# Kernel tuning notes

Measured on AMD Instinct MI355X. Metric: run time of the kernel, lower is better.

Reference implementation:

```python
import jax, jax.numpy as jnp
import numpy as np


def log_g(x):
    # faithful to torch: where(x>=0, log(relu(x)+0.5), 5 - softplus(-x))
    return jnp.where(x >= 0, jnp.log(jax.nn.relu(x) + 0.5), 5.0 - jax.nn.softplus(-x))


def setup_inputs() -> dict:
    key = jax.random.key(0)
    ks = jax.random.split(key, 6)
    B, T, D, H = 8, 4096, 1024, 1024
    s = 1.0 / np.sqrt(D)
    return {
        "x": jax.random.normal(ks[0], (B, T, D), jnp.float32),
        "h_0": jax.random.normal(ks[1], (B, 1, H), jnp.float32),
        "Wz_w": jax.random.normal(ks[2], (D, H), jnp.float32) * s,
        "Wz_b": jax.random.normal(ks[3], (H,), jnp.float32) * 0.1,
        "Wh_w": jax.random.normal(ks[4], (D, H), jnp.float32) * s,
        "Wh_b": jax.random.normal(ks[5], (H,), jnp.float32) * 0.1,
    }


def reference(x, h_0, Wz_w, Wz_b, Wh_w, Wh_b):
    # k = W_z(x)
    k = jnp.einsum('btd,dh->bth', x, Wz_w) + Wz_b
    log_z = -jax.nn.softplus(-k)          # log sigmoid(k)
    log_coeffs = -jax.nn.softplus(k)      # log(1 - sigmoid(k))
    log_h0 = log_g(h_0)                                            # [B,1,H]
    log_tilde_h = log_g(jnp.einsum('btd,dh->bth', x, Wh_w) + Wh_b)  # [B,T,H]
    log_values = jnp.concatenate([log_h0, log_z + log_tilde_h], axis=1)  # [B,T+1,H]
    # a_star = pad(cumsum(log_coeffs, dim=1), (0,0,1,0)) -> one zero row at t=0
    a_star = jnp.pad(jnp.cumsum(log_coeffs, axis=1), ((0, 0), (1, 0), (0, 0)))  # [B,T+1,H]
    log_h = a_star + jax.lax.cumlogsumexp(log_values - a_star, axis=1)
    return jnp.exp(log_h)[:, 1:]  # [B,T,H]
```

## Files before the change

### kernel.cpp

```cpp
#include <hip/hip_runtime.h>
#include <hip/hip_bf16.h>
#include <stdint.h>

#define B_   8
#define T_   4096
#define D_   1024
#define H_   1024
#define M_   (B_ * T_)
#define NC_  64
#define TC_  64


typedef __attribute__((ext_vector_type(4))) float f32x4;
typedef __attribute__((ext_vector_type(8))) short bfr8;
typedef _Float16 f16;
typedef __attribute__((ext_vector_type(2))) _Float16 f16x2;

__device__ __forceinline__ unsigned short f2bf(float f) {
  unsigned int u = __float_as_uint(f);
  u += 0x7fffu + ((u >> 16) & 1u);
  return (unsigned short)(u >> 16);
}
__device__ __forceinline__ float bf2f(unsigned short h) {
  return __uint_as_float(((unsigned int)h) << 16);
}

__device__ __forceinline__ void gload16(const void* g, void* l) {
  __builtin_amdgcn_global_load_lds((const __attribute__((address_space(1))) void*)g,
                                   (__attribute__((address_space(3))) void*)l,
                                   16, 0, 0);
}

__device__ __forceinline__ float g_of(float hv) {
  return (hv >= 0.f) ? (hv + 0.5f)
                     : 148.4131591025766f / (1.f + __expf(-hv));
}

__global__ void prep_w2(const float* __restrict__ Wz, const float* __restrict__ Wh,
                        unsigned short* __restrict__ wtp, float* __restrict__ whT,
                        unsigned int* __restrict__ fcnt)
{
  int kt = blockIdx.x;
  int nt = blockIdx.y;
  int m  = blockIdx.z;
  if (kt == 0 && nt == 0 && m == 0 && threadIdx.x == 0) *fcnt = 0u;
  __shared__ float tile[32][65];
  const float* W = m ? Wh : Wz;
  int n0 = nt * 64, k0 = kt * 32;
  int t = threadIdx.x;
  {
    int r = t >> 3, c0 = (t & 7) * 8;
    const float* src = &W[(size_t)(k0 + r) * 1024 + n0 + c0];
#pragma unroll
    for (int i = 0; i < 8; i++) tile[r][c0 + i] = src[i];
  }
  __syncthreads();
  unsigned short* out = wtp + ((size_t)(m * 16 + nt) * 32 + kt) * 4096;
  {
    int n = t >> 2;
    int cb = (t & 3) * 2;
    unsigned int u[8];
#pragma unroll
    for (int q = 0; q < 8; q++) {
      unsigned short w2[2];
#pragma unroll
      for (int h = 0; h < 2; h++) {
        int e = q * 2 + h;
        int c = cb + (e >> 3), el = e & 7;
        int s = c ^ (n & 7);
        float v = tile[(s & 3) * 8 + el][n];
        unsigned short hi = f2bf(v);
        w2[h] = (s < 4) ? hi : f2bf(v - bf2f(hi));
      }
      u[q] = (unsigned int)w2[0] | ((unsigned int)w2[1] << 16);
    }
    uint4* dst = (uint4*)&out[(size_t)n * 64 + cb * 8];
    dst[0] = make_uint4(u[0], u[1], u[2], u[3]);
    dst[1] = make_uint4(u[4], u[5], u[6], u[7]);
  }
  if (m == 1) {
    int n = t >> 2, kk0 = (t & 3) * 8;
    float* dstf = &whT[(size_t)(n0 + n) * 1024 + k0 + kk0];
#pragma unroll
    for (int i = 0; i < 8; i++) dstf[i] = tile[kk0 + i][n];
  }
}

__global__ __launch_bounds__(256, 2) void gemm_cv(
    const float* __restrict__ x,
    const unsigned short* __restrict__ wtp,
    const float* __restrict__ bz, const float* __restrict__ bhb,
    f16x2* __restrict__ cvbuf,
    unsigned int* __restrict__ fcnt, unsigned int* __restrict__ flist,
    unsigned int fcap)
{
  __shared__ __align__(16) unsigned short Ac[2][8192];
  __shared__ __align__(16) unsigned short Bzs[2][4096];
  __shared__ __align__(16) unsigned short Bhs[2][4096];
  int tid = threadIdx.x;
  int lane = tid & 63, wv = tid >> 6;
  int wr = wv >> 1, wc = wv & 1;
  int lrow = lane & 15, lq = lane >> 4;

  int bid = blockIdx.x;
  int cpx = gridDim.x >> 3;
  int swz = (bid & 7) * cpx + (bid >> 3);
  int grp = swz >> 7, wi = swz & 127;
  int mt = grp * 8 + (wi & 7);
  int nt = wi >> 3;
  int m0 = mt * 128, n0 = nt * 64;

  f32x4 accz[4][2], acch[4][2];
#pragma unroll
  for (int i = 0; i < 4; i++)
#pragma unroll
    for (int j = 0; j < 2; j++) {
      accz[i][j] = (f32x4){0.f, 0.f, 0.f, 0.f};
      acch[i][j] = (f32x4){0.f, 0.f, 0.f, 0.f};
    }

  int art = tid >> 3, ac4 = (tid & 7) * 4;
  int awb = art * 64 + ((((ac4 >> 3) ^ (art & 7)) << 3) | (ac4 & 4));
  const float* xp = x + (size_t)(m0 + art) * D_ + ac4;

  int fch = (lq ^ (lrow & 7)) << 3;
  int aoff = (wr * 64 + lrow) * 64 + fch;
  int boff = (wc * 32 + lrow) * 64 + fch;

  const unsigned short* bsz = wtp + (size_t)nt * 131072 + tid * 8;
  const unsigned short* bsh = bsz + 2097152;

  uint4 xa[4];

  auto loadX = [&](int kt) {
#pragma unroll
    for (int p = 0; p < 4; p++)
      xa[p] = *(const uint4*)(xp + (size_t)p * 32 * D_ + kt * 32);
  };
  auto stageB = [&](int kt, int b) {
#pragma unroll
    for (int j = 0; j < 2; j++) {
      gload16(bsz + (size_t)kt * 4096 + j * 2048, &Bzs[b][j * 2048 + tid * 8]);
      gload16(bsh + (size_t)kt * 4096 + j * 2048, &Bhs[b][j * 2048 + tid * 8]);
    }
  };
  auto writeA = [&](int b) {
#pragma unroll
    for (int p = 0; p < 4; p++) {
      uint4 vu = xa[p];
      unsigned int hi01 = __builtin_amdgcn_perm(vu.y, vu.x, 0x07060302u);
      unsigned int hi23 = __builtin_amdgcn_perm(vu.w, vu.z, 0x07060302u);
      float l0 = __uint_as_float(vu.x) - __uint_as_float(vu.x & 0xffff0000u);
      float l1 = __uint_as_float(vu.y) - __uint_as_float(vu.y & 0xffff0000u);
      float l2 = __uint_as_float(vu.z) - __uint_as_float(vu.z & 0xffff0000u);
      float l3 = __uint_as_float(vu.w) - __uint_as_float(vu.w & 0xffff0000u);
      unsigned int lo01 = __builtin_amdgcn_perm(__float_as_uint(l1),
                                                __float_as_uint(l0), 0x07060302u);
      unsigned int lo23 = __builtin_amdgcn_perm(__float_as_uint(l3),
                                                __float_as_uint(l2), 0x07060302u);
      int bi = p * 2048 + awb;
      *(uint2*)&Ac[b][bi]      = make_uint2(hi01, hi23);
      *(uint2*)&Ac[b][bi ^ 32] = make_uint2(lo01, lo23);
    }
  };
  auto doMFMA = [&](int cur) {
    bfr8 ah[4], al[4], bzhv[2], bzlv[2], bhhv[2], bhlv[2];
#pragma unroll
    for (int f = 0; f < 4; f++) {
      ah[f] = *(const bfr8*)&Ac[cur][aoff + f * 1024];
      al[f] = *(const bfr8*)&Ac[cur][(aoff + f * 1024) ^ 32];
    }
#pragma unroll
    for (int j = 0; j < 2; j++) {
      bzhv[j] = *(const bfr8*)&Bzs[cur][boff + j * 1024];
      bzlv[j] = *(const bfr8*)&Bzs[cur][(boff + j * 1024) ^ 32];
      bhhv[j] = *(const bfr8*)&Bhs[cur][boff + j * 1024];
      bhlv[j] = *(const bfr8*)&Bhs[cur][(boff + j * 1024) ^ 32];
    }
#pragma unroll
    for (int i = 0; i < 4; i++)
#pragma unroll
      for (int j = 0; j < 2; j++) {
        accz[i][j] = __builtin_amdgcn_mfma_f32_16x16x32_bf16(ah[i], bzhv[j], accz[i][j], 0, 0, 0);
        accz[i][j] = __builtin_amdgcn_mfma_f32_16x16x32_bf16(al[i], bzhv[j], accz[i][j], 0, 0, 0);
        accz[i][j] = __builtin_amdgcn_mfma_f32_16x16x32_bf16(ah[i], bzlv[j], accz[i][j], 0, 0, 0);
        acch[i][j] = __builtin_amdgcn_mfma_f32_16x16x32_bf16(ah[i], bhhv[j], acch[i][j], 0, 0, 0);
        acch[i][j] = __builtin_amdgcn_mfma_f32_16x16x32_bf16(al[i], bhhv[j], acch[i][j], 0, 0, 0);
        acch[i][j] = __builtin_amdgcn_mfma_f32_16x16x32_bf16(ah[i], bhlv[j], acch[i][j], 0, 0, 0);
      }
  };

  loadX(0);
  stageB(0, 0);
  writeA(0);
  __syncthreads();

  auto step = [&](int kt, int cur, int nxt) {
    loadX(kt + 1);
    stageB(kt + 1, nxt);
    doMFMA(cur);
    writeA(nxt);
    __syncthreads();
  };

#pragma unroll 1
  for (int kt = 0; kt < 30; kt += 2) {
    step(kt, 0, 1);
    step(kt + 1, 1, 0);
  }
  step(30, 0, 1);
  doMFMA(1);

#pragma unroll
  for (int j = 0; j < 2; j++) {
    int col = n0 + wc * 32 + j * 16 + lrow;
    float kb = bz[col], hb = bhb[col];
#pragma unroll
    for (int i = 0; i < 4; i++) {
      int row0 = m0 + wr * 64 + i * 16 + lq * 4;
#pragma unroll
      for (int r = 0; r < 4; r++) {
        float kv = accz[i][j][r] + kb;
        float hv = acch[i][j][r] + hb;
        f16 kf = (f16)kv;
        float c  = 1.f / (1.f + __expf((float)kf));
        float v  = (1.f - c) * g_of(hv);
        size_t off = (size_t)(row0 + r) * H_ + col;
        f16x2 pr; pr[0] = kf; pr[1] = (f16)v;
        cvbuf[off] = pr;
        if (__builtin_fabsf(hv) < 1e-3f) {
          unsigned int p = atomicAdd(fcnt, 1u);
          if (p < fcap) flist[p] = (unsigned int)off;
        }
      }
    }
  }
}

__global__ void fixup_kc512(const float* __restrict__ x, const float* __restrict__ whT,
                            const float* __restrict__ bhb, f16x2* cvbuf,
                            const unsigned int* __restrict__ fcnt,
                            const unsigned int* __restrict__ flist, unsigned int fcap)
{
  unsigned int n = *fcnt; if (n > fcap) n = fcap;
  unsigned int gtid = blockIdx.x * blockDim.x + threadIdx.x;
  unsigned int nt = gridDim.x * blockDim.x;
  const unsigned int lim = (unsigned int)M_ * (unsigned int)H_;
  for (unsigned int i = gtid; i < n; i += nt) {
    unsigned int o = flist[i];
    if (o >= lim) continue;
    unsigned int row = o >> 10, col = o & 1023u;
    const float* xr = x + (size_t)row * D_;
    const float* wr = whT + (size_t)col * D_;
    float a1 = 0.f, a2 = 0.f;
    for (int d = 0; d < 512; d++)
      a1 = fmaf(xr[d], wr[d], a1);
    for (int d = 512; d < 1024; d++)
      a2 = fmaf(xr[d], wr[d], a2);
    float hs = (a1 + a2) + bhb[col];
    float g  = (hs >= 0.f) ? (hs + 0.5f)
                           : 148.4131591025766f / (1.f + __expf(-hs));
    f16x2 pr = cvbuf[o];
    float z  = 1.f / (1.f + __expf(-(float)pr[0]));
    pr[1] = (f16)(z * g);
    cvbuf[o] = pr;
  }
}

__global__ void scan_p1(const f16x2* __restrict__ cv,
                        float* __restrict__ Cc, float* __restrict__ Vv)
{
  int h = blockIdx.x * 256 + threadIdx.x;
  int ch = blockIdx.y, b = blockIdx.z;
  size_t base = ((size_t)b * T_ + (size_t)ch * TC_) * H_ + h;
  float C = 1.f, V = 0.f;
#pragma unroll 4
  for (int i = 0; i < TC_; i++) {
    f16x2 p = cv[base + (size_t)i * H_];
    float c = 1.f / (1.f + __expf((float)p[0]));
    V = fmaf(c, V, (float)p[1]);
    C *= c;
  }
  size_t o = ((size_t)b * NC_ + ch) * H_ + h;
  Cc[o] = C; Vv[o] = V;
}

__global__ void scan_p2(const float* __restrict__ h0, const float* __restrict__ Cc,
                        const float* __restrict__ Vv, float* __restrict__ Hi)
{
  int idx = blockIdx.x * 256 + threadIdx.x;
  float hs = g_of(h0[idx]);
  int b = idx >> 10, h = idx & 1023;
  for (int ch = 0; ch < NC_; ch++) {
    size_t o = ((size_t)b * NC_ + ch) * H_ + h;
    Hi[o] = hs;
    hs = fmaf(Cc[o], hs, Vv[o]);
  }
}

__global__ void scan_p3(void* buf, const float* __restrict__ Hi)
{
  __shared__ f16x2 S[TC_][256];
  const f16x2* cv = (const f16x2*)buf;
  float* out = (float*)buf;
  int t = threadIdx.x;
  int hg = blockIdx.x, ch = blockIdx.y, b = blockIdx.z;
  int col = hg * 256 + t;
  size_t base = ((size_t)b * T_ + (size_t)ch * TC_) * H_ + col;
#pragma unroll 4
  for (int r = 0; r < TC_; r++)
    S[r][t] = cv[base + (size_t)r * H_];
  __syncthreads();
  float hs = Hi[((size_t)b * NC_ + ch) * H_ + col];
#pragma unroll 4
  for (int r = 0; r < TC_; r++) {
    f16x2 p = S[r][t];
    float c = 1.f / (1.f + __expf((float)p[0]));
    hs = fmaf(c, hs, (float)p[1]);
    out[base + (size_t)r * H_] = hs;
  }
}

extern "C" void kernel_launch(void* const* d_in, const int* in_sizes, int n_in,
                              void* d_out, int out_size, void* d_ws, size_t ws_size,
                              hipStream_t stream)
{
  const float* x  = (const float*)d_in[0];
  const float* h0 = (const float*)d_in[1];
  const float* Wz = (const float*)d_in[2];
  const float* bz = (const float*)d_in[3];
  const float* Wh = (const float*)d_in[4];
  const float* bh = (const float*)d_in[5];
  char* ws = (char*)d_ws;

  const size_t MiB = 1024u * 1024u;
  unsigned int* fcnt  = (unsigned int*)(ws);
  unsigned int* flist = (unsigned int*)(ws + 4096);
  const unsigned int fcap = 250u * 1024u;
  unsigned short* wtp = (unsigned short*)(ws + 2 * MiB);
  float* Cc = (float*)(ws + 10 * MiB);
  float* Vv = (float*)(ws + 12 * MiB);
  float* Hi = (float*)(ws + 14 * MiB);
  float* whT = (float*)(ws + 16 * MiB);

  f16x2* cvbuf = (f16x2*)d_out;

  prep_w2<<<dim3(32, 16, 2), 256, 0, stream>>>(Wz, Wh, wtp, whT, fcnt);
  gemm_cv<<<4096, 256, 0, stream>>>(x, wtp, bz, bh, cvbuf, fcnt, flist, fcap);
  fixup_kc512<<<512, 256, 0, stream>>>(x, whT, bh, cvbuf, fcnt, flist, fcap);
  scan_p1<<<dim3(4, 64, 8), 256, 0, stream>>>(cvbuf, Cc, Vv);
  scan_p2<<<32, 256, 0, stream>>>(h0, Cc, Vv, Hi);
  scan_p3<<<dim3(4, 64, 8), 256, 0, stream>>>(d_out, Hi);
}
```

Measured before the change: 708.0 us.

## Enlarge GEMM block tile to 256x128 with 8 waves and raise MFMA priority

The main GEMM moves from 128x64 tiles with 4 waves to 256x128 tiles with 8 waves (512 threads). The weight prep kernel is reworked to emit matching 128-column packed tiles. The goal is more reuse of the split-bf16 A and B operands per LDS load and less global traffic per output element. The change also adds s_setprio around the MFMA loop and swaps __syncthreads for an explicit waitcnt plus barrier. In exchange it uses more LDS and accumulator registers per block, which may lower occupancy, and the grid shrinks to 1024 blocks.

```diff
diff --git a/kernel.cpp b/kernel.cpp
--- a/kernel.cpp
+++ b/kernel.cpp
@@ -44,49 +44,46 @@
   int nt = blockIdx.y;
   int m  = blockIdx.z;
   if (kt == 0 && nt == 0 && m == 0 && threadIdx.x == 0) *fcnt = 0u;
-  __shared__ float tile[32][65];
+  __shared__ float tile[32][129];
   const float* W = m ? Wh : Wz;
-  int n0 = nt * 64, k0 = kt * 32;
+  int n0 = nt * 128, k0 = kt * 32;
   int t = threadIdx.x;
   {
-    int r = t >> 3, c0 = (t & 7) * 8;
+    int r = t >> 3, c0 = (t & 7) * 16;
     const float* src = &W[(size_t)(k0 + r) * 1024 + n0 + c0];
 #pragma unroll
-    for (int i = 0; i < 8; i++) tile[r][c0 + i] = src[i];
+    for (int i = 0; i < 16; i++) tile[r][c0 + i] = src[i];
   }
   __syncthreads();
-  unsigned short* out = wtp + ((size_t)(m * 16 + nt) * 32 + kt) * 4096;
-  {
-    int n = t >> 2;
-    int cb = (t & 3) * 2;
-    unsigned int u[8];
-#pragma unroll
-    for (int q = 0; q < 8; q++) {
+  unsigned short* out = wtp + ((size_t)(m * 8 + nt) * 32 + kt) * 8192;
+  int n = t >> 1, hf = t & 1;
+#pragma unroll
+  for (int c4 = 0; c4 < 4; c4++) {
+    int c = hf * 4 + c4;
+    int s = c ^ (n & 7);
+    unsigned int u[4];
+#pragma unroll
+    for (int q = 0; q < 4; q++) {
       unsigned short w2[2];
 #pragma unroll
-      for (int h = 0; h < 2; h++) {
-        int e = q * 2 + h;
-        int c = cb + (e >> 3), el = e & 7;
-        int s = c ^ (n & 7);
-        float v = tile[(s & 3) * 8 + el][n];
+      for (int e2 = 0; e2 < 2; e2++) {
+        int e = q * 2 + e2;
+        float v = tile[(s & 3) * 8 + e][n];
         unsigned short hi = f2bf(v);
-        w2[h] = (s < 4) ? hi : f2bf(v - bf2f(hi));
+        w2[e2] = (s < 4) ? hi : f2bf(v - bf2f(hi));
       }
       u[q] = (unsigned int)w2[0] | ((unsigned int)w2[1] << 16);
     }
-    uint4* dst = (uint4*)&out[(size_t)n * 64 + cb * 8];
-    dst[0] = make_uint4(u[0], u[1], u[2], u[3]);
-    dst[1] = make_uint4(u[4], u[5], u[6], u[7]);
+    *(uint4*)&out[(size_t)n * 64 + c * 8] = make_uint4(u[0], u[1], u[2], u[3]);
   }
   if (m == 1) {
-    int n = t >> 2, kk0 = (t & 3) * 8;
-    float* dstf = &whT[(size_t)(n0 + n) * 1024 + k0 + kk0];
-#pragma unroll
-    for (int i = 0; i < 8; i++) dstf[i] = tile[kk0 + i][n];
-  }
-}
-
-__global__ __launch_bounds__(256, 2) void gemm_cv(
+#pragma unroll
+    for (int i = 0; i < 16; i++)
+      whT[(size_t)(n0 + n) * 1024 + k0 + hf * 16 + i] = tile[hf * 16 + i][n];
+  }
+}
+
+__global__ __launch_bounds__(512, 2) void gemm_cv(
     const float* __restrict__ x,
     const unsigned short* __restrict__ wtp,
     const float* __restrict__ bz, const float* __restrict__ bhb,
@@ -94,130 +91,162 @@
     unsigned int* __restrict__ fcnt, unsigned int* __restrict__ flist,
     unsigned int fcap)
 {
-  __shared__ __align__(16) unsigned short Ac[2][8192];
-  __shared__ __align__(16) unsigned short Bzs[2][4096];
-  __shared__ __align__(16) unsigned short Bhs[2][4096];
+  __shared__ __align__(16) unsigned short Ac[2][16384];
+  __shared__ __align__(16) unsigned short Bz[2][8192];
+  __shared__ __align__(16) unsigned short Bh[2][8192];
   int tid = threadIdx.x;
   int lane = tid & 63, wv = tid >> 6;
-  int wr = wv >> 1, wc = wv & 1;
+  int wm = wv >> 2, wn = wv & 3;
   int lrow = lane & 15, lq = lane >> 4;
 
   int bid = blockIdx.x;
   int cpx = gridDim.x >> 3;
   int swz = (bid & 7) * cpx + (bid >> 3);
-  int grp = swz >> 7, wi = swz & 127;
-  int mt = grp * 8 + (wi & 7);
-  int nt = wi >> 3;
-  int m0 = mt * 128, n0 = nt * 64;
-
-  f32x4 accz[4][2], acch[4][2];
-#pragma unroll
-  for (int i = 0; i < 4; i++)
+  int nt = swz & 7;
+  int mt = swz >> 3;
+  int m0 = mt * 256, n0 = nt * 128;
+
+  f32x4 accz[8][2], acch[8][2];
+#pragma unroll
+  for (int i = 0; i < 8; i++)
 #pragma unroll
     for (int j = 0; j < 2; j++) {
       accz[i][j] = (f32x4){0.f, 0.f, 0.f, 0.f};
       acch[i][j] = (f32x4){0.f, 0.f, 0.f, 0.f};
     }
 
-  int art = tid >> 3, ac4 = (tid & 7) * 4;
-  int awb = art * 64 + ((((ac4 >> 3) ^ (art & 7)) << 3) | (ac4 & 4));
-  const float* xp = x + (size_t)(m0 + art) * D_ + ac4;
+  int art = tid >> 1, half = tid & 1;
+  int r7 = art & 7;
+  int c0 = (((half * 2)     ) ^ r7) << 3;
+  int c1 = (((half * 2) + 1) ^ r7) << 3;
+  int abw = art * 64;
+  const float* xp = x + (size_t)(m0 + art) * D_ + half * 16;
 
   int fch = (lq ^ (lrow & 7)) << 3;
-  int aoff = (wr * 64 + lrow) * 64 + fch;
-  int boff = (wc * 32 + lrow) * 64 + fch;
-
-  const unsigned short* bsz = wtp + (size_t)nt * 131072 + tid * 8;
+  int abase = (wm * 128 + lrow) * 64 + fch;
+  int bbase = (wn * 32 + lrow) * 64 + fch;
+
+  const unsigned short* bsz = wtp + (size_t)nt * 262144;
   const unsigned short* bsh = bsz + 2097152;
 
   uint4 xa[4];
 
   auto loadX = [&](int kt) {
 #pragma unroll
-    for (int p = 0; p < 4; p++)
-      xa[p] = *(const uint4*)(xp + (size_t)p * 32 * D_ + kt * 32);
-  };
-  auto stageB = [&](int kt, int b) {
+    for (int q = 0; q < 4; q++)
+      xa[q] = *(const uint4*)(xp + (size_t)kt * 32 + q * 4);
+  };
+  auto stageB = [&](int kt, int nb) {
+    size_t o = (size_t)kt * 8192 + tid * 8;
+    gload16(bsz + o,        &Bz[nb][tid * 8]);
+    gload16(bsz + o + 4096, &Bz[nb][4096 + tid * 8]);
+    gload16(bsh + o,        &Bh[nb][tid * 8]);
+    gload16(bsh + o + 4096, &Bh[nb][4096 + tid * 8]);
+  };
+  auto writeA = [&](int nb) {
+    unsigned int h00 = __builtin_amdgcn_perm(xa[0].y, xa[0].x, 0x07060302u);
+    unsigned int h01 = __builtin_amdgcn_perm(xa[0].w, xa[0].z, 0x07060302u);
+    unsigned int h02 = __builtin_amdgcn_perm(xa[1].y, xa[1].x, 0x07060302u);
+    unsigned int h03 = __builtin_amdgcn_perm(xa[1].w, xa[1].z, 0x07060302u);
+    unsigned int h10 = __builtin_amdgcn_perm(xa[2].y, xa[2].x, 0x07060302u);
+    unsigned int h11 = __builtin_amdgcn_perm(xa[2].w, xa[2].z, 0x07060302u);
+    unsigned int h12 = __builtin_amdgcn_perm(xa[3].y, xa[3].x, 0x07060302u);
+    unsigned int h13 = __builtin_amdgcn_perm(xa[3].w, xa[3].z, 0x07060302u);
+    unsigned int l00, l01, l02, l03, l10, l11, l12, l13;
+    {
+      float a0 = __uint_as_float(xa[0].x) - __uint_as_float(xa[0].x & 0xffff0000u);
+      float a1 = __uint_as_float(xa[0].y) - __uint_as_float(xa[0].y & 0xffff0000u);
+      float a2 = __uint_as_float(xa[0].z) - __uint_as_float(xa[0].z & 0xffff0000u);
+      float a3 = __uint_as_float(xa[0].w) - __uint_as_float(xa[0].w & 0xffff0000u);
+      float b0 = __uint_as_float(xa[1].x) - __uint_as_float(xa[1].x & 0xffff0000u);
+      float b1 = __uint_as_float(xa[1].y) - __uint_as_float(xa[1].y & 0xffff0000u);
+      float b2 = __uint_as_float(xa[1].z) - __uint_as_float(xa[1].z & 0xffff0000u);
+      float b3 = __uint_as_float(xa[1].w) - __uint_as_float(xa[1].w & 0xffff0000u);
+      l00 = __builtin_amdgcn_perm(__float_as_uint(a1), __float_as_uint(a0), 0x07060302u);
+      l01 = __builtin_amdgcn_perm(__float_as_uint(a3), __float_as_uint(a2), 0x07060302u);
+      l02 = __builtin_amdgcn_perm(__float_as_uint(b1), __float_as_uint(b0), 0x07060302u);
+      l03 = __builtin_amdgcn_perm(__float_as_uint(b3), __float_as_uint(b2), 0x07060302u);
+    }
+    {
+      float a0 = __uint_as_float(xa[2].x) - __uint_as_float(xa[2].x & 0xffff0000u);
+      float a1 = __uint_as_float(xa[2].y) - __uint_as_float(xa[2].y & 0xffff0000u);
+      float a2 = __uint_as_float(xa[2].z) - __uint_as_float(xa[2].z & 0xffff0000u);
+      float a3 = __uint_as_float(xa[2].w) - __uint_as_float(xa[2].w & 0xffff0000u);
+      float b0 = __uint_as_float(xa[3].x) - __uint_as_float(xa[3].x & 0xffff0000u);
+      float b1 = __uint_as_float(xa[3].y) - __uint_as_float(xa[3].y & 0xffff0000u);
+      float b2 = __uint_as_float(xa[3].z) - __uint_as_float(xa[3].z & 0xffff0000u);
+      float b3 = __uint_as_float(xa[3].w) - __uint_as_float(xa[3].w & 0xffff0000u);
+      l10 = __builtin_amdgcn_perm(__float_as_uint(a1), __float_as_uint(a0), 0x07060302u);
+      l11 = __builtin_amdgcn_perm(__float_as_uint(a3), __float_as_uint(a2), 0x07060302u);
+      l12 = __builtin_amdgcn_perm(__float_as_uint(b1), __float_as_uint(b0), 0x07060302u);
+      l13 = __builtin_amdgcn_perm(__float_as_uint(b3), __float_as_uint(b2), 0x07060302u);
+    }
+    *(uint4*)&Ac[nb][abw + c0]        = make_uint4(h00, h01, h02, h03);
+    *(uint4*)&Ac[nb][abw + c1]        = make_uint4(h10, h11, h12, h13);
+    *(uint4*)&Ac[nb][(abw + c0) ^ 32] = make_uint4(l00, l01, l02, l03);
+    *(uint4*)&Ac[nb][(abw + c1) ^ 32] = make_uint4(l10, l11, l12, l13);
+  };
+  auto mfma_tile = [&](int cur) {
+    bfr8 bzh[2], bzl[2], bhh[2], bhl[2];
 #pragma unroll
     for (int j = 0; j < 2; j++) {
-      gload16(bsz + (size_t)kt * 4096 + j * 2048, &Bzs[b][j * 2048 + tid * 8]);
-      gload16(bsh + (size_t)kt * 4096 + j * 2048, &Bhs[b][j * 2048 + tid * 8]);
-    }
-  };
-  auto writeA = [&](int b) {
-#pragma unroll
-    for (int p = 0; p < 4; p++) {
-      uint4 vu = xa[p];
-      unsigned int hi01 = __builtin_amdgcn_perm(vu.y, vu.x, 0x07060302u);
-      unsigned int hi23 = __builtin_amdgcn_perm(vu.w, vu.z, 0x07060302u);
-      float l0 = __uint_as_float(vu.x) - __uint_as_float(vu.x & 0xffff0000u);
-      float l1 = __uint_as_float(vu.y) - __uint_as_float(vu.y & 0xffff0000u);
-      float l2 = __uint_as_float(vu.z) - __uint_as_float(vu.z & 0xffff0000u);
-      float l3 = __uint_as_float(vu.w) - __uint_as_float(vu.w & 0xffff0000u);
-      unsigned int lo01 = __builtin_amdgcn_perm(__float_as_uint(l1),
-                                                __float_as_uint(l0), 0x07060302u);
-      unsigned int lo23 = __builtin_amdgcn_perm(__float_as_uint(l3),
-                                                __float_as_uint(l2), 0x07060302u);
-      int bi = p * 2048 + awb;
-      *(uint2*)&Ac[b][bi]      = make_uint2(hi01, hi23);
-      *(uint2*)&Ac[b][bi ^ 32] = make_uint2(lo01, lo23);
-    }
-  };
-  auto doMFMA = [&](int cur) {
-    bfr8 ah[4], al[4], bzhv[2], bzlv[2], bhhv[2], bhlv[2];
-#pragma unroll
-    for (int f = 0; f < 4; f++) {
-      ah[f] = *(const bfr8*)&Ac[cur][aoff + f * 1024];
-      al[f] = *(const bfr8*)&Ac[cur][(aoff + f * 1024) ^ 32];
-    }
-#pragma unroll
-    for (int j = 0; j < 2; j++) {
-      bzhv[j] = *(const bfr8*)&Bzs[cur][boff + j * 1024];
-      bzlv[j] = *(const bfr8*)&Bzs[cur][(boff + j * 1024) ^ 32];
-      bhhv[j] = *(const bfr8*)&Bhs[cur][boff + j * 1024];
-      bhlv[j] = *(const bfr8*)&Bhs[cur][(boff + j * 1024) ^ 32];
-    }
-#pragma unroll
-    for (int i = 0; i < 4; i++)
+      int o = bbase + j * 1024;
+      bzh[j] = *(const bfr8*)&Bz[cur][o];
+      bzl[j] = *(const bfr8*)&Bz[cur][o ^ 32];
+      bhh[j] = *(const bfr8*)&Bh[cur][o];
+      bhl[j] = *(const bfr8*)&Bh[cur][o ^ 32];
+    }
+    __builtin_amdgcn_s_setprio(1);
+#pragma unroll
+    for (int i = 0; i < 8; i++) {
+      int o = abase + i * 1024;
+      bfr8 ah = *(const bfr8*)&Ac[cur][o];
+      bfr8 al = *(const bfr8*)&Ac[cur][o ^ 32];
 #pragma unroll
       for (int j = 0; j < 2; j++) {
-        accz[i][j] = __builtin_amdgcn_mfma_f32_16x16x32_bf16(ah[i], bzhv[j], accz[i][j], 0, 0, 0);
-        accz[i][j] = __builtin_amdgcn_mfma_f32_16x16x32_bf16(al[i], bzhv[j], accz[i][j], 0, 0, 0);
-        accz[i][j] = __builtin_amdgcn_mfma_f32_16x16x32_bf16(ah[i], bzlv[j], accz[i][j], 0, 0, 0);
-        acch[i][j] = __builtin_amdgcn_mfma_f32_16x16x32_bf16(ah[i], bhhv[j], acch[i][j], 0, 0, 0);
-        acch[i][j] = __builtin_amdgcn_mfma_f32_16x16x32_bf16(al[i], bhhv[j], acch[i][j], 0, 0, 0);
-        acch[i][j] = __builtin_amdgcn_mfma_f32_16x16x32_bf16(ah[i], bhlv[j], acch[i][j], 0, 0, 0);
+        accz[i][j] = __builtin_amdgcn_mfma_f32_16x16x32_bf16(ah, bzh[j], accz[i][j], 0, 0, 0);
+        accz[i][j] = __builtin_amdgcn_mfma_f32_16x16x32_bf16(al, bzh[j], accz[i][j], 0, 0, 0);
+        accz[i][j] = __builtin_amdgcn_mfma_f32_16x16x32_bf16(ah, bzl[j], accz[i][j], 0, 0, 0);
+        acch[i][j] = __builtin_amdgcn_mfma_f32_16x16x32_bf16(ah, bhh[j], acch[i][j], 0, 0, 0);
+        acch[i][j] = __builtin_amdgcn_mfma_f32_16x16x32_bf16(al, bhh[j], acch[i][j], 0, 0, 0);
+        acch[i][j] = __builtin_amdgcn_mfma_f32_16x16x32_bf16(ah, bhl[j], acch[i][j], 0, 0, 0);
       }
+    }
+    __builtin_amdgcn_s_setprio(0);
   };
 
   loadX(0);
   stageB(0, 0);
   writeA(0);
-  __syncthreads();
-
-  auto step = [&](int kt, int cur, int nxt) {
+  asm volatile("s_waitcnt vmcnt(0) lgkmcnt(0)" ::: "memory");
+  __builtin_amdgcn_sched_barrier(0);
+  __builtin_amdgcn_s_barrier();
+
+  auto kstep = [&](int kt, int cur) {
     loadX(kt + 1);
-    stageB(kt + 1, nxt);
-    doMFMA(cur);
-    writeA(nxt);
-    __syncthreads();
+    stageB(kt + 1, cur ^ 1);
+    mfma_tile(cur);
+    writeA(cur ^ 1);
+    asm volatile("s_waitcnt vmcnt(0) lgkmcnt(0)" ::: "memory");
+    __builtin_amdgcn_sched_barrier(0);
+    __builtin_amdgcn_s_barrier();
   };
 
 #pragma unroll 1
   for (int kt = 0; kt < 30; kt += 2) {
-    step(kt, 0, 1);
-    step(kt + 1, 1, 0);
-  }
-  step(30, 0, 1);
-  doMFMA(1);
+    kstep(kt, 0);
+    kstep(kt + 1, 1);
+  }
+  kstep(30, 0);
+  mfma_tile(1);
 
 #pragma unroll
   for (int j = 0; j < 2; j++) {
-    int col = n0 + wc * 32 + j * 16 + lrow;
+    int col = n0 + wn * 32 + j * 16 + lrow;
     float kb = bz[col], hb = bhb[col];
 #pragma unroll
-    for (int i = 0; i < 4; i++) {
-      int row0 = m0 + wr * 64 + i * 16 + lq * 4;
+    for (int i = 0; i < 8; i++) {
+      int row0 = m0 + wm * 128 + i * 16 + lq * 4;
 #pragma unroll
       for (int r = 0; r < 4; r++) {
         float kv = accz[i][j][r] + kb;
@@ -345,8 +374,8 @@
 
   f16x2* cvbuf = (f16x2*)d_out;
 
-  prep_w2<<<dim3(32, 16, 2), 256, 0, stream>>>(Wz, Wh, wtp, whT, fcnt);
-  gemm_cv<<<4096, 256, 0, stream>>>(x, wtp, bz, bh, cvbuf, fcnt, flist, fcap);
+  prep_w2<<<dim3(32, 8, 2), 256, 0, stream>>>(Wz, Wh, wtp, whT, fcnt);
+  gemm_cv<<<1024, 512, 0, stream>>>(x, wtp, bz, bh, cvbuf, fcnt, flist, fcap);
   fixup_kc512<<<512, 256, 0, stream>>>(x, whT, bh, cvbuf, fcnt, flist, fcap);
   scan_p1<<<dim3(4, 64, 8), 256, 0, stream>>>(cvbuf, Cc, Vv);
   scan_p2<<<32, 256, 0, stream>>>(h0, Cc, Vv, Hi);
```

Result: slower. 747.2 us (+5.5%).

## Replace double-buffered LDS pipeline with single buffer and two barriers per k-step

Applied to the files above, without the earlier changes.

The GEMM main loop drops its double-buffered shared-memory tiles for A and B in favor of single buffers, issuing B staging and the A write, syncing, prefetching the next X into registers, running MFMAs, then syncing again. This halves LDS use per block, which can allow more resident blocks per CU. In exchange it adds a second barrier per iteration and loses the overlap between filling the next buffer and computing on the current one, so global-to-LDS B loads are now exposed.

```diff
diff --git a/kernel.cpp b/kernel.cpp
--- a/kernel.cpp
+++ b/kernel.cpp
@@ -94,9 +94,9 @@
     unsigned int* __restrict__ fcnt, unsigned int* __restrict__ flist,
     unsigned int fcap)
 {
-  __shared__ __align__(16) unsigned short Ac[2][8192];
-  __shared__ __align__(16) unsigned short Bzs[2][4096];
-  __shared__ __align__(16) unsigned short Bhs[2][4096];
+  __shared__ __align__(16) unsigned short Ac[8192];
+  __shared__ __align__(16) unsigned short Bzs[4096];
+  __shared__ __align__(16) unsigned short Bhs[4096];
   int tid = threadIdx.x;
   int lane = tid & 63, wv = tid >> 6;
   int wr = wv >> 1, wc = wv & 1;
@@ -137,14 +137,14 @@
     for (int p = 0; p < 4; p++)
       xa[p] = *(const uint4*)(xp + (size_t)p * 32 * D_ + kt * 32);
   };
-  auto stageB = [&](int kt, int b) {
-#pragma unroll
-    for (int j = 0; j < 2; j++) {
-      gload16(bsz + (size_t)kt * 4096 + j * 2048, &Bzs[b][j * 2048 + tid * 8]);
-      gload16(bsh + (size_t)kt * 4096 + j * 2048, &Bhs[b][j * 2048 + tid * 8]);
-    }
+  auto stageB = [&](int kt) {
+    size_t o = (size_t)kt * 4096;
+    gload16(bsz + o,        &Bzs[tid * 8]);
+    gload16(bsz + o + 2048, &Bzs[2048 + tid * 8]);
+    gload16(bsh + o,        &Bhs[tid * 8]);
+    gload16(bsh + o + 2048, &Bhs[2048 + tid * 8]);
   };
-  auto writeA = [&](int b) {
+  auto writeA = [&]() {
 #pragma unroll
     for (int p = 0; p < 4; p++) {
       uint4 vu = xa[p];
@@ -159,57 +159,49 @@
       unsigned int lo23 = __builtin_amdgcn_perm(__float_as_uint(l3),
                                                 __float_as_uint(l2), 0x07060302u);
       int bi = p * 2048 + awb;
-      *(uint2*)&Ac[b][bi]      = make_uint2(hi01, hi23);
-      *(uint2*)&Ac[b][bi ^ 32] = make_uint2(lo01, lo23);
+      *(uint2*)&Ac[bi]      = make_uint2(hi01, hi23);
+      *(uint2*)&Ac[bi ^ 32] = make_uint2(lo01, lo23);
     }
   };
-  auto doMFMA = [&](int cur) {
-    bfr8 ah[4], al[4], bzhv[2], bzlv[2], bhhv[2], bhlv[2];
+  auto doMFMA = [&]() {
+    bfr8 ah[4], al[4], bzh[2], bzl[2], bhh[2], bhl[2];
 #pragma unroll
     for (int f = 0; f < 4; f++) {
-      ah[f] = *(const bfr8*)&Ac[cur][aoff + f * 1024];
-      al[f] = *(const bfr8*)&Ac[cur][(aoff + f * 1024) ^ 32];
+      int o = aoff + f * 1024;
+      ah[f] = *(const bfr8*)&Ac[o];
+      al[f] = *(const bfr8*)&Ac[o ^ 32];
     }
 #pragma unroll
     for (int j = 0; j < 2; j++) {
-      bzhv[j] = *(const bfr8*)&Bzs[cur][boff + j * 1024];
-      bzlv[j] = *(const bfr8*)&Bzs[cur][(boff + j * 1024) ^ 32];
-      bhhv[j] = *(const bfr8*)&Bhs[cur][boff + j * 1024];
-      bhlv[j] = *(const bfr8*)&Bhs[cur][(boff + j * 1024) ^ 32];
+      int o = boff + j * 1024;
+      bzh[j] = *(const bfr8*)&Bzs[o];
+      bzl[j] = *(const bfr8*)&Bzs[o ^ 32];
+      bhh[j] = *(const bfr8*)&Bhs[o];
+      bhl[j] = *(const bfr8*)&Bhs[o ^ 32];
     }
 #pragma unroll
     for (int i = 0; i < 4; i++)
 #pragma unroll
       for (int j = 0; j < 2; j++) {
-        accz[i][j] = __builtin_amdgcn_mfma_f32_16x16x32_bf16(ah[i], bzhv[j], accz[i][j], 0, 0, 0);
-        accz[i][j] = __builtin_amdgcn_mfma_f32_16x16x32_bf16(al[i], bzhv[j], accz[i][j], 0, 0, 0);
-        accz[i][j] = __builtin_amdgcn_mfma_f32_16x16x32_bf16(ah[i], bzlv[j], accz[i][j], 0, 0, 0);
-        acch[i][j] = __builtin_amdgcn_mfma_f32_16x16x32_bf16(ah[i], bhhv[j], acch[i][j], 0, 0, 0);
-        acch[i][j] = __builtin_amdgcn_mfma_f32_16x16x32_bf16(al[i], bhhv[j], acch[i][j], 0, 0, 0);
-        acch[i][j] = __builtin_amdgcn_mfma_f32_16x16x32_bf16(ah[i], bhlv[j], acch[i][j], 0, 0, 0);
+        accz[i][j] = __builtin_amdgcn_mfma_f32_16x16x32_bf16(ah[i], bzh[j], accz[i][j], 0, 0, 0);
+        accz[i][j] = __builtin_amdgcn_mfma_f32_16x16x32_bf16(al[i], bzh[j], accz[i][j], 0, 0, 0);
+        accz[i][j] = __builtin_amdgcn_mfma_f32_16x16x32_bf16(ah[i], bzl[j], accz[i][j], 0, 0, 0);
+        acch[i][j] = __builtin_amdgcn_mfma_f32_16x16x32_bf16(ah[i], bhh[j], acch[i][j], 0, 0, 0);
+        acch[i][j] = __builtin_amdgcn_mfma_f32_16x16x32_bf16(al[i], bhh[j], acch[i][j], 0, 0, 0);
+        acch[i][j] = __builtin_amdgcn_mfma_f32_16x16x32_bf16(ah[i], bhl[j], acch[i][j], 0, 0, 0);
       }
   };
 
   loadX(0);
-  stageB(0, 0);
-  writeA(0);
-  __syncthreads();
-
-  auto step = [&](int kt, int cur, int nxt) {
-    loadX(kt + 1);
-    stageB(kt + 1, nxt);
-    doMFMA(cur);
-    writeA(nxt);
+#pragma unroll 1
+  for (int kt = 0; kt < 32; ++kt) {
+    stageB(kt);
+    writeA();
     __syncthreads();
-  };
-
-#pragma unroll 1
-  for (int kt = 0; kt < 30; kt += 2) {
-    step(kt, 0, 1);
-    step(kt + 1, 1, 0);
-  }
-  step(30, 0, 1);
-  doMFMA(1);
+    if (kt < 31) loadX(kt + 1);
+    doMFMA();
+    if (kt < 31) __syncthreads();
+  }
 
 #pragma unroll
   for (int j = 0; j < 2; j++) {
```

New measurement: 677.8 us. 1.04x faster.
